# Kernel tuning notes

Hardware: AMD Instinct MI355X
Metric: run time of the kernel (lower is better)

## Reference

```python
import jax, jax.numpy as jnp
import numpy as np
import math

DIMS = 128
VOXEL_SIZE = 4.0
QUANT_SIZE = 0.02
QUANT_LEN = int((2 * VOXEL_SIZE + 0.0001) // QUANT_SIZE)  # 400
N = 1024


def setup_inputs() -> dict:
    key = jax.random.key(0)
    k1, k2, k3, k4, k5, k6 = jax.random.split(key, 6)
    features = jax.random.normal(k1, (N, DIMS), dtype=jnp.float32)
    # distances uniform in [-voxel_size, voxel_size)
    voxel_distances = (jax.random.uniform(k2, (N, N, 3), dtype=jnp.float32) * 2.0 - 1.0) * VOXEL_SIZE
    W_qkv = jax.random.normal(k3, (DIMS, 3 * DIMS), dtype=jnp.float32) * 0.02
    b_qkv = jnp.zeros((3 * DIMS,), dtype=jnp.float32)
    table_x = jax.random.normal(k4, (3, QUANT_LEN, DIMS), dtype=jnp.float32) * 0.02
    table_y = jax.random.normal(k5, (3, QUANT_LEN, DIMS), dtype=jnp.float32) * 0.02
    table_z = jax.random.normal(k6, (3, QUANT_LEN, DIMS), dtype=jnp.float32) * 0.02
    return {"features": features, "voxel_distances": voxel_distances,
            "W_qkv": W_qkv, "b_qkv": b_qkv,
            "table_x": table_x, "table_y": table_y, "table_z": table_z}


def reference(features, voxel_distances, W_qkv, b_qkv, table_x, table_y, table_z):
    n, dims = features.shape
    qkv = (features @ W_qkv + b_qkv).reshape(n, 3, dims)
    q, k, v = qkv[:, 0], qkv[:, 1], qkv[:, 2]  # each [N, D]

    # quantized distance indices, clamped like torch's .clamp(max=...)
    max_idx = VOXEL_SIZE * 2.0 / QUANT_SIZE - 1.0  # 399
    idx = jnp.floor((voxel_distances + VOXEL_SIZE) / QUANT_SIZE)
    idx = jnp.clip(idx, 0.0, max_idx).astype(jnp.int32)  # [N, N, 3]

    # gathered positional encoding: [N, N, D]
    encode_k = table_x[1][idx[:, :, 0]] + table_y[1][idx[:, :, 1]] + table_z[1][idx[:, :, 2]]
    # bias[i, j] = k[i] . encode_k[i, j]  (faithful to k[:, None] @ encode_k^T)
    position_bias = jnp.einsum('id,ijd->ij', k, encode_k)

    scores = (q @ k.T + position_bias) / math.sqrt(dims)
    attn = jax.nn.softmax(scores, axis=-1)  # [N, N]
    return attn @ v  # [N, D]
```

## Files before the change

kernel.cpp:

```cpp
#include <hip/hip_runtime.h>
#include <math.h>

#define N_PTS 1024
#define D 128
#define QL 400
#define PLD 1200
#define SQRT_D_INV 0.08838834764831845f

typedef __attribute__((ext_vector_type(8))) short bf16x8;
typedef __attribute__((ext_vector_type(4))) float f32x4;
typedef unsigned short u16;

#define GLOBAL_AS __attribute__((address_space(1)))
#define LDS_AS    __attribute__((address_space(3)))

__device__ __forceinline__ u16 f2bf(float x) {
    union { float f; unsigned u; } v; v.f = x;
    unsigned r = v.u + 0x7fff + ((v.u >> 16) & 1);
    return (u16)(r >> 16);
}
__device__ __forceinline__ float b2f(u16 h) {
    union { unsigned u; float f; } v; v.u = ((unsigned)h) << 16;
    return v.f;
}

__global__ __launch_bounds__(256) void prep2_kernel(
    const float* __restrict__ features, const float* __restrict__ W,
    const float* __restrict__ bias,
    const float* __restrict__ tx, const float* __restrict__ ty,
    const float* __restrict__ tz,
    u16* __restrict__ qb, u16* __restrict__ kb, u16* __restrict__ vT,
    u16* __restrict__ Pb, unsigned* __restrict__ cnt)
{
    __shared__ __align__(16) u16 smem[24704];
    const int tid = threadIdx.x;
    const int bx = blockIdx.x;
    const int wave = tid >> 6, lane = tid & 63;
    const int wr = wave >> 1, wc = wave & 1;
    const int l15 = lane & 15, l4 = lane >> 4;

    if (bx == 0 && tid < 64) cnt[tid] = 0u;

    if (bx < 96) {
        u16* As = smem;
        u16* Bs = smem + 8192;
        const int bm = (bx / 6) * 64;
        const int bn = (bx % 6) * 64;

        #pragma unroll
        for (int r0 = 0; r0 < 4; ++r0) {
            int unit = r0 * 256 + tid;
            int row = unit >> 4, c16 = unit & 15;
            const float* ga = features + (size_t)(bm + row) * D + c16 * 8;
            float4 a0 = *(const float4*)ga;
            float4 a1 = *(const float4*)(ga + 4);
            u16 h[8] = {f2bf(a0.x), f2bf(a0.y), f2bf(a0.z), f2bf(a0.w),
                        f2bf(a1.x), f2bf(a1.y), f2bf(a1.z), f2bf(a1.w)};
            *(bf16x8*)(As + row * 128 + ((c16 ^ (row & 7)) * 8)) = *(bf16x8*)h;
        }
        #pragma unroll
        for (int r2 = 0; r2 < 8; ++r2) {
            int k = r2 * 16 + (tid >> 4);
            int nl = (tid & 15) * 4;
            float4 w4 = *(const float4*)&W[(size_t)k * 384 + bn + nl];
            float wv[4] = {w4.x, w4.y, w4.z, w4.w};
            #pragma unroll
            for (int e = 0; e < 4; ++e) {
                int n = nl + e;
                Bs[n * 128 + (((k >> 3) ^ (n & 7)) << 3) + (k & 7)] = f2bf(wv[e]);
            }
        }
        __syncthreads();

        f32x4 acc[2][2] = {};
        #pragma unroll
        for (int ks = 0; ks < 4; ++ks) {
            bf16x8 a[2], b[2];
            #pragma unroll
            for (int m = 0; m < 2; ++m) {
                int row = wr * 32 + m * 16 + l15;
                int c16 = ks * 4 + l4;
                a[m] = *(const bf16x8*)(As + row * 128 + ((c16 ^ (row & 7)) * 8));
            }
            #pragma unroll
            for (int n = 0; n < 2; ++n) {
                int row = wc * 32 + n * 16 + l15;
                int c16 = ks * 4 + l4;
                b[n] = *(const bf16x8*)(Bs + row * 128 + ((c16 ^ (row & 7)) * 8));
            }
            #pragma unroll
            for (int m = 0; m < 2; ++m)
                #pragma unroll
                for (int n = 0; n < 2; ++n)
                    acc[m][n] = __builtin_amdgcn_mfma_f32_16x16x32_bf16(
                        a[m], b[n], acc[m][n], 0, 0, 0);
        }

        #pragma unroll
        for (int m = 0; m < 2; ++m)
            #pragma unroll
            for (int n = 0; n < 2; ++n)
                #pragma unroll
                for (int r = 0; r < 4; ++r) {
                    int grow = bm + wr * 32 + m * 16 + l4 * 4 + r;
                    int gcol = bn + wc * 32 + n * 16 + l15;
                    float val = acc[m][n][r] + bias[gcol];
                    int reg = gcol >> 7, lc = gcol & 127;
                    if (reg == 0)      qb[grow * D + lc] = f2bf(val * SQRT_D_INV);
                    else if (reg == 1) kb[grow * D + lc] = f2bf(val);
                    else               vT[(size_t)lc * N_PTS + grow] = f2bf(val);
                }
        return;
    }

    const int t = bx - 96;
    const int ib = t / 19, jb = t % 19;
    const int bm = ib * 64, bn = jb * 64;
    u16* Ta = smem;
    u16* Wb = smem + 8192;
    float* bPl = (float*)(smem + 24576);

    #pragma unroll
    for (int r0 = 0; r0 < 4; ++r0) {
        int unit = r0 * 256 + tid;
        int row = unit >> 4, c16 = unit & 15;
        int c = bn + row; if (c > PLD - 1) c = PLD - 1;
        int sec = c / QL, rr = c - sec * QL;
        const float* tsec = (sec == 0) ? tx : ((sec == 1) ? ty : tz);
        const float* ga = tsec + QL * D + rr * D + c16 * 8;
        float4 a0 = *(const float4*)ga;
        float4 a1 = *(const float4*)(ga + 4);
        u16 h[8] = {f2bf(a0.x), f2bf(a0.y), f2bf(a0.z), f2bf(a0.w),
                    f2bf(a1.x), f2bf(a1.y), f2bf(a1.z), f2bf(a1.w)};
        *(bf16x8*)(Ta + row * 128 + ((c16 ^ (row & 7)) * 8)) = *(bf16x8*)h;
    }
    #pragma unroll
    for (int r0 = 0; r0 < 8; ++r0) {
        int unit = r0 * 256 + tid;
        int e = unit >> 4, c16 = unit & 15;
        const float* ga = W + (size_t)e * 384 + 128 + c16 * 8;
        float4 a0 = *(const float4*)ga;
        float4 a1 = *(const float4*)(ga + 4);
        u16 h[8] = {f2bf(a0.x), f2bf(a0.y), f2bf(a0.z), f2bf(a0.w),
                    f2bf(a1.x), f2bf(a1.y), f2bf(a1.z), f2bf(a1.w)};
        *(bf16x8*)(Wb + e * 128 + ((c16 ^ (e & 7)) * 8)) = *(bf16x8*)h;
    }
    __syncthreads();

    f32x4 accG[2][4] = {};
    #pragma unroll
    for (int ks = 0; ks < 4; ++ks) {
        bf16x8 a[2], bfr[4];
        #pragma unroll
        for (int m = 0; m < 2; ++m) {
            int row = wr * 32 + m * 16 + l15;
            int c16 = ks * 4 + l4;
            a[m] = *(const bf16x8*)(Ta + row * 128 + ((c16 ^ (row & 7)) * 8));
        }
        #pragma unroll
        for (int n = 0; n < 4; ++n) {
            int e = wc * 64 + n * 16 + l15;
            int c16 = ks * 4 + l4;
            bfr[n] = *(const bf16x8*)(Wb + e * 128 + ((c16 ^ (e & 7)) * 8));
        }
        #pragma unroll
        for (int m = 0; m < 2; ++m)
            #pragma unroll
            for (int n = 0; n < 4; ++n)
                accG[m][n] = __builtin_amdgcn_mfma_f32_16x16x32_bf16(
                    a[m], bfr[n], accG[m][n], 0, 0, 0);
    }

    float bsum = 0.0f;
    {
        int c_l = tid >> 2, q = tid & 3;
        #pragma unroll
        for (int dd = 0; dd < 32; ++dd) {
            int d = q * 32 + dd;
            u16 tv = Ta[c_l * 128 + (((d >> 3) ^ (c_l & 7)) * 8) + (d & 7)];
            bsum += b2f(tv) * bias[128 + d];
        }
        bsum += __shfl_xor(bsum, 1);
        bsum += __shfl_xor(bsum, 2);
    }
    __syncthreads();

    #pragma unroll
    for (int m = 0; m < 2; ++m)
        #pragma unroll
        for (int n = 0; n < 4; ++n)
            #pragma unroll
            for (int rr = 0; rr < 4; ++rr) {
                int c_l = wr * 32 + m * 16 + l4 * 4 + rr;
                int e   = wc * 64 + n * 16 + l15;
                Wb[c_l * 128 + (((e >> 3) ^ (c_l & 7)) * 8) + (e & 7)] =
                    f2bf(accG[m][n][rr]);
            }
    #pragma unroll
    for (int r0 = 0; r0 < 4; ++r0) {
        int unit = r0 * 256 + tid;
        int row = unit >> 4, c16 = unit & 15;
        const float* ga = features + (size_t)(bm + row) * D + c16 * 8;
        float4 a0 = *(const float4*)ga;
        float4 a1 = *(const float4*)(ga + 4);
        u16 h[8] = {f2bf(a0.x), f2bf(a0.y), f2bf(a0.z), f2bf(a0.w),
                    f2bf(a1.x), f2bf(a1.y), f2bf(a1.z), f2bf(a1.w)};
        *(bf16x8*)(Ta + row * 128 + ((c16 ^ (row & 7)) * 8)) = *(bf16x8*)h;
    }
    if ((tid & 3) == 0) bPl[tid >> 2] = bsum;
    __syncthreads();

    f32x4 acc[2][2] = {};
    #pragma unroll
    for (int ks = 0; ks < 4; ++ks) {
        bf16x8 a[2], bq[2];
        #pragma unroll
        for (int m = 0; m < 2; ++m) {
            int row = wr * 32 + m * 16 + l15;
            int c16 = ks * 4 + l4;
            a[m] = *(const bf16x8*)(Ta + row * 128 + ((c16 ^ (row & 7)) * 8));
        }
        #pragma unroll
        for (int n = 0; n < 2; ++n) {
            int crow = wc * 32 + n * 16 + l15;
            int c16 = ks * 4 + l4;
            bq[n] = *(const bf16x8*)(Wb + crow * 128 + ((c16 ^ (crow & 7)) * 8));
        }
        #pragma unroll
        for (int m = 0; m < 2; ++m)
            #pragma unroll
            for (int n = 0; n < 2; ++n)
                acc[m][n] = __builtin_amdgcn_mfma_f32_16x16x32_bf16(
                    a[m], bq[n], acc[m][n], 0, 0, 0);
    }
    #pragma unroll
    for (int m = 0; m < 2; ++m)
        #pragma unroll
        for (int n = 0; n < 2; ++n)
            #pragma unroll
            for (int rr = 0; rr < 4; ++rr) {
                int grow = bm + wr * 32 + m * 16 + l4 * 4 + rr;
                int gcol = bn + wc * 32 + n * 16 + l15;
                int c_l  = wc * 32 + n * 16 + l15;
                if (gcol < PLD)
                    Pb[(size_t)grow * PLD + gcol] =
                        f2bf((acc[m][n][rr] + bPl[c_l]) * SQRT_D_INV);
            }
}

__global__ __launch_bounds__(256) void flash_kernel(
    const u16* __restrict__ qb,
    const u16* __restrict__ kb,
    const u16* __restrict__ vT,
    const u16* __restrict__ Pb,
    const float* __restrict__ vd,
    float* __restrict__ part,
    float* __restrict__ rowsumC,
    unsigned* __restrict__ cnt,
    float* __restrict__ out)
{
    __shared__ __align__(16) u16 Pl[2432 * 8];
    __shared__ __align__(16) u16 Ps[16 * 128];
    __shared__ float rsw[4][16];
    __shared__ int lastflag;
    const int tid = threadIdx.x;
    const int wave = tid >> 6, lane = tid & 63;
    const int l15 = lane & 15, l4 = lane >> 4;
    const int it = blockIdx.x;
    const int chunk = blockIdx.y;
    const int bm = it * 16;
    const int bn = chunk * 128;

    const u16* Pg = Pb + (size_t)bm * PLD;
    #pragma unroll
    for (int r0 = 0; r0 < 9; ++r0) {
        int unit = r0 * 256 + tid;
        __builtin_amdgcn_global_load_lds(
            (const GLOBAL_AS unsigned int*)(Pg + unit * 8),
            (LDS_AS unsigned int*)(Pl + r0 * 2048 + wave * 512), 16, 0, 0);
    }
    if (wave < 2) {
        int unit = 9 * 256 + tid;
        int cu = unit > 2399 ? 2399 : unit;
        __builtin_amdgcn_global_load_lds(
            (const GLOBAL_AS unsigned int*)(Pg + cu * 8),
            (LDS_AS unsigned int*)(Pl + 9 * 2048 + wave * 512), 16, 0, 0);
    }

    float vx[2][4], vy[2][4], vz[2][4];
    #pragma unroll
    for (int nn = 0; nn < 2; ++nn)
        #pragma unroll
        for (int r = 0; r < 4; ++r) {
            int i = l4 * 4 + r;
            int j = wave * 32 + nn * 16 + l15;
            const float* vp = vd + ((size_t)(bm + i) * N_PTS + bn + j) * 3;
            vx[nn][r] = vp[0]; vy[nn][r] = vp[1]; vz[nn][r] = vp[2];
        }

    bf16x8 aq[4];
    #pragma unroll
    for (int ks = 0; ks < 4; ++ks)
        aq[ks] = *(const bf16x8*)(qb + (size_t)(bm + l15) * D + ks * 32 + l4 * 8);
    f32x4 acc[2] = {};
    #pragma unroll
    for (int nn = 0; nn < 2; ++nn) {
        int jt = bn + wave * 32 + nn * 16;
        #pragma unroll
        for (int ks = 0; ks < 4; ++ks) {
            bf16x8 bk = *(const bf16x8*)(kb + (size_t)(jt + l15) * D + ks * 32 + l4 * 8);
            acc[nn] = __builtin_amdgcn_mfma_f32_16x16x32_bf16(aq[ks], bk, acc[nn], 0, 0, 0);
        }
    }
    __syncthreads();

    float rs[4] = {0.f, 0.f, 0.f, 0.f};
    #pragma unroll
    for (int nn = 0; nn < 2; ++nn)
        #pragma unroll
        for (int r = 0; r < 4; ++r) {
            int i = l4 * 4 + r;
            int jl = wave * 32 + nn * 16 + l15;
            int ix = (int)floorf((vx[nn][r] + 4.0f) * 50.0f);
            int iy = (int)floorf((vy[nn][r] + 4.0f) * 50.0f);
            int iz = (int)floorf((vz[nn][r] + 4.0f) * 50.0f);
            ix = min(max(ix, 0), QL - 1);
            iy = min(max(iy, 0), QL - 1);
            iz = min(max(iz, 0), QL - 1);
            const u16* Pr = Pl + i * PLD;
            float bv = b2f(Pr[ix]) + b2f(Pr[QL + iy]) + b2f(Pr[2 * QL + iz]);
            float e = __expf(acc[nn][r] + bv);
            rs[r] += e;
            Ps[i * 128 + (((jl >> 3) ^ (i & 7)) * 8) + (jl & 7)] = f2bf(e);
        }
    #pragma unroll
    for (int r = 0; r < 4; ++r)
        #pragma unroll
        for (int off = 1; off < 16; off <<= 1)
            rs[r] += __shfl_xor(rs[r], off);
    if (l15 == 0)
        #pragma unroll
        for (int r = 0; r < 4; ++r) rsw[wave][l4 * 4 + r] = rs[r];
    __syncthreads();
    if (tid < 16)
        rowsumC[(it * 8 + chunk) * 16 + tid] =
            rsw[0][tid] + rsw[1][tid] + rsw[2][tid] + rsw[3][tid];

    bf16x8 pa[4];
    #pragma unroll
    for (int kt = 0; kt < 4; ++kt)
        pa[kt] = *(const bf16x8*)(Ps + l15 * 128 + (((kt * 4 + l4) ^ (l15 & 7)) * 8));
    f32x4 acc2[2] = {};
    #pragma unroll
    for (int nn = 0; nn < 2; ++nn) {
        int dt = wave * 32 + nn * 16;
        #pragma unroll
        for (int kt = 0; kt < 4; ++kt) {
            bf16x8 bv8 = *(const bf16x8*)(vT + (size_t)(dt + l15) * N_PTS + bn + kt * 32 + l4 * 8);
            acc2[nn] = __builtin_amdgcn_mfma_f32_16x16x32_bf16(pa[kt], bv8, acc2[nn], 0, 0, 0);
        }
    }
    float* po = part + (size_t)(it * 8 + chunk) * (16 * D);
    #pragma unroll
    for (int nn = 0; nn < 2; ++nn)
        #pragma unroll
        for (int r = 0; r < 4; ++r)
            po[(l4 * 4 + r) * D + wave * 32 + nn * 16 + l15] = acc2[nn][r];

    asm volatile("s_waitcnt vmcnt(0)" ::: "memory");
    __syncthreads();
    if (tid == 0) {
        unsigned old = __hip_atomic_fetch_add(
            &cnt[it], 1u, __ATOMIC_RELAXED, __HIP_MEMORY_SCOPE_AGENT);
        lastflag = (old == 7u);
    }
    __syncthreads();
    if (lastflag) {
        const float4* p4 = (const float4*)(part + (size_t)it * 8 * 16 * D);
        const float* rsb = rowsumC + it * 8 * 16;
        #pragma unroll
        for (int h = 0; h < 2; ++h) {
            int f4 = h * 256 + tid;
            int row = f4 >> 5;
            float rsum = 0.0f;
            #pragma unroll
            for (int z = 0; z < 8; ++z) rsum += rsb[z * 16 + row];
            float inv = 1.0f / rsum;
            float4 a = p4[f4];
            #pragma unroll
            for (int z = 1; z < 8; ++z) {
                float4 v = p4[z * 512 + f4];
                a.x += v.x; a.y += v.y; a.z += v.z; a.w += v.w;
            }
            a.x *= inv; a.y *= inv; a.z *= inv; a.w *= inv;
            ((float4*)out)[bm * 32 + f4] = a;
        }
    }
}

extern "C" void kernel_launch(void* const* d_in, const int* in_sizes, int n_in,
                              void* d_out, int out_size, void* d_ws, size_t ws_size,
                              hipStream_t stream)
{
    const float* features = (const float*)d_in[0];
    const float* vd       = (const float*)d_in[1];
    const float* W        = (const float*)d_in[2];
    const float* b        = (const float*)d_in[3];
    const float* tx       = (const float*)d_in[4];
    const float* ty       = (const float*)d_in[5];
    const float* tz       = (const float*)d_in[6];
    float* out = (float*)d_out;

    char* w0 = (char*)d_ws;
    unsigned* cnt = (unsigned*)w0;
    u16* qb       = (u16*)(w0 + 0x1000);
    u16* kb       = (u16*)(w0 + 0x50000);
    u16* vT       = (u16*)(w0 + 0x90000);
    u16* Pb       = (u16*)(w0 + 0xD0000);
    float* part   = (float*)(w0 + 0x330000);
    float* rowsumC= (float*)(w0 + 0x730000);

    dim3 blk(256);

    prep2_kernel<<<dim3(400), blk, 0, stream>>>(
        features, W, b, tx, ty, tz, qb, kb, vT, Pb, cnt);

    flash_kernel<<<dim3(64, 8), blk, 0, stream>>>(
        qb, kb, vT, Pb, vd, part, rowsumC, cnt, out);
}
```

Baseline: 23.85 us.

## Double waves per flash block and halve QKV GEMM tile rows

```diff
diff --git a/kernel.cpp b/kernel.cpp
--- a/kernel.cpp
+++ b/kernel.cpp
@@ -41,14 +41,14 @@
 
     if (bx == 0 && tid < 64) cnt[tid] = 0u;
 
-    if (bx < 96) {
+    if (bx < 192) {
         u16* As = smem;
-        u16* Bs = smem + 8192;
-        const int bm = (bx / 6) * 64;
+        u16* Bs = smem + 4096;
+        const int bm = (bx / 6) * 32;
         const int bn = (bx % 6) * 64;
 
         #pragma unroll
-        for (int r0 = 0; r0 < 4; ++r0) {
+        for (int r0 = 0; r0 < 2; ++r0) {
             int unit = r0 * 256 + tid;
             int row = unit >> 4, c16 = unit & 15;
             const float* ga = features + (size_t)(bm + row) * D + c16 * 8;
@@ -72,48 +72,40 @@
         }
         __syncthreads();
 
-        f32x4 acc[2][2] = {};
+        f32x4 acc[2] = {};
         #pragma unroll
         for (int ks = 0; ks < 4; ++ks) {
-            bf16x8 a[2], b[2];
-            #pragma unroll
-            for (int m = 0; m < 2; ++m) {
-                int row = wr * 32 + m * 16 + l15;
-                int c16 = ks * 4 + l4;
-                a[m] = *(const bf16x8*)(As + row * 128 + ((c16 ^ (row & 7)) * 8));
-            }
+            bf16x8 a, b[2];
+            int arow = wr * 16 + l15;
+            int c16 = ks * 4 + l4;
+            a = *(const bf16x8*)(As + arow * 128 + ((c16 ^ (arow & 7)) * 8));
             #pragma unroll
             for (int n = 0; n < 2; ++n) {
                 int row = wc * 32 + n * 16 + l15;
-                int c16 = ks * 4 + l4;
                 b[n] = *(const bf16x8*)(Bs + row * 128 + ((c16 ^ (row & 7)) * 8));
             }
             #pragma unroll
-            for (int m = 0; m < 2; ++m)
-                #pragma unroll
-                for (int n = 0; n < 2; ++n)
-                    acc[m][n] = __builtin_amdgcn_mfma_f32_16x16x32_bf16(
-                        a[m], b[n], acc[m][n], 0, 0, 0);
-        }
-
-        #pragma unroll
-        for (int m = 0; m < 2; ++m)
-            #pragma unroll
             for (int n = 0; n < 2; ++n)
-                #pragma unroll
-                for (int r = 0; r < 4; ++r) {
-                    int grow = bm + wr * 32 + m * 16 + l4 * 4 + r;
-                    int gcol = bn + wc * 32 + n * 16 + l15;
-                    float val = acc[m][n][r] + bias[gcol];
-                    int reg = gcol >> 7, lc = gcol & 127;
-                    if (reg == 0)      qb[grow * D + lc] = f2bf(val * SQRT_D_INV);
-                    else if (reg == 1) kb[grow * D + lc] = f2bf(val);
-                    else               vT[(size_t)lc * N_PTS + grow] = f2bf(val);
-                }
+                acc[n] = __builtin_amdgcn_mfma_f32_16x16x32_bf16(
+                    a, b[n], acc[n], 0, 0, 0);
+        }
+
+        #pragma unroll
+        for (int n = 0; n < 2; ++n)
+            #pragma unroll
+            for (int r = 0; r < 4; ++r) {
+                int grow = bm + wr * 16 + l4 * 4 + r;
+                int gcol = bn + wc * 32 + n * 16 + l15;
+                float val = acc[n][r] + bias[gcol];
+                int reg = gcol >> 7, lc = gcol & 127;
+                if (reg == 0)      qb[grow * D + lc] = f2bf(val * SQRT_D_INV);
+                else if (reg == 1) kb[grow * D + lc] = f2bf(val);
+                else               vT[(size_t)lc * N_PTS + grow] = f2bf(val);
+            }
         return;
     }
 
-    const int t = bx - 96;
+    const int t = bx - 192;
     const int ib = t / 19, jb = t % 19;
     const int bm = ib * 64, bn = jb * 64;
     u16* Ta = smem;
@@ -248,7 +240,7 @@
             }
 }
 
-__global__ __launch_bounds__(256) void flash_kernel(
+__global__ __launch_bounds__(512) void flash_kernel(
     const u16* __restrict__ qb,
     const u16* __restrict__ kb,
     const u16* __restrict__ vT,
@@ -259,12 +251,12 @@
     unsigned* __restrict__ cnt,
     float* __restrict__ out)
 {
-    __shared__ __align__(16) u16 Pl[2432 * 8];
+    __shared__ __align__(16) u16 Pl[2560 * 8];
     __shared__ __align__(16) u16 Ps[16 * 128];
-    __shared__ float rsw[4][16];
+    __shared__ float rsw[8][16];
     __shared__ int lastflag;
     const int tid = threadIdx.x;
-    const int wave = tid >> 6, lane = tid & 63;
+    const int w = tid >> 6, lane = tid & 63;
     const int l15 = lane & 15, l4 = lane >> 4;
     const int it = blockIdx.x;
     const int chunk = blockIdx.y;
@@ -273,66 +265,55 @@
 
     const u16* Pg = Pb + (size_t)bm * PLD;
     #pragma unroll
-    for (int r0 = 0; r0 < 9; ++r0) {
-        int unit = r0 * 256 + tid;
-        __builtin_amdgcn_global_load_lds(
-            (const GLOBAL_AS unsigned int*)(Pg + unit * 8),
-            (LDS_AS unsigned int*)(Pl + r0 * 2048 + wave * 512), 16, 0, 0);
-    }
-    if (wave < 2) {
-        int unit = 9 * 256 + tid;
+    for (int r0 = 0; r0 < 5; ++r0) {
+        int unit = r0 * 512 + tid;
         int cu = unit > 2399 ? 2399 : unit;
         __builtin_amdgcn_global_load_lds(
             (const GLOBAL_AS unsigned int*)(Pg + cu * 8),
-            (LDS_AS unsigned int*)(Pl + 9 * 2048 + wave * 512), 16, 0, 0);
-    }
-
-    float vx[2][4], vy[2][4], vz[2][4];
-    #pragma unroll
-    for (int nn = 0; nn < 2; ++nn)
-        #pragma unroll
-        for (int r = 0; r < 4; ++r) {
-            int i = l4 * 4 + r;
-            int j = wave * 32 + nn * 16 + l15;
-            const float* vp = vd + ((size_t)(bm + i) * N_PTS + bn + j) * 3;
-            vx[nn][r] = vp[0]; vy[nn][r] = vp[1]; vz[nn][r] = vp[2];
-        }
+            (LDS_AS unsigned int*)(Pl + r0 * 4096 + w * 512), 16, 0, 0);
+    }
+
+    float vx[4], vy[4], vz[4];
+    #pragma unroll
+    for (int r = 0; r < 4; ++r) {
+        int i = l4 * 4 + r;
+        int j = bn + w * 16 + l15;
+        const float* vp = vd + ((size_t)(bm + i) * N_PTS + j) * 3;
+        vx[r] = vp[0]; vy[r] = vp[1]; vz[r] = vp[2];
+    }
 
     bf16x8 aq[4];
     #pragma unroll
     for (int ks = 0; ks < 4; ++ks)
         aq[ks] = *(const bf16x8*)(qb + (size_t)(bm + l15) * D + ks * 32 + l4 * 8);
-    f32x4 acc[2] = {};
-    #pragma unroll
-    for (int nn = 0; nn < 2; ++nn) {
-        int jt = bn + wave * 32 + nn * 16;
+    f32x4 acc = {};
+    {
+        int jt = bn + w * 16;
         #pragma unroll
         for (int ks = 0; ks < 4; ++ks) {
             bf16x8 bk = *(const bf16x8*)(kb + (size_t)(jt + l15) * D + ks * 32 + l4 * 8);
-            acc[nn] = __builtin_amdgcn_mfma_f32_16x16x32_bf16(aq[ks], bk, acc[nn], 0, 0, 0);
-        }
-    }
-    __syncthreads();
-
-    float rs[4] = {0.f, 0.f, 0.f, 0.f};
-    #pragma unroll
-    for (int nn = 0; nn < 2; ++nn)
-        #pragma unroll
-        for (int r = 0; r < 4; ++r) {
-            int i = l4 * 4 + r;
-            int jl = wave * 32 + nn * 16 + l15;
-            int ix = (int)floorf((vx[nn][r] + 4.0f) * 50.0f);
-            int iy = (int)floorf((vy[nn][r] + 4.0f) * 50.0f);
-            int iz = (int)floorf((vz[nn][r] + 4.0f) * 50.0f);
-            ix = min(max(ix, 0), QL - 1);
-            iy = min(max(iy, 0), QL - 1);
-            iz = min(max(iz, 0), QL - 1);
-            const u16* Pr = Pl + i * PLD;
-            float bv = b2f(Pr[ix]) + b2f(Pr[QL + iy]) + b2f(Pr[2 * QL + iz]);
-            float e = __expf(acc[nn][r] + bv);
-            rs[r] += e;
-            Ps[i * 128 + (((jl >> 3) ^ (i & 7)) * 8) + (jl & 7)] = f2bf(e);
-        }
+            acc = __builtin_amdgcn_mfma_f32_16x16x32_bf16(aq[ks], bk, acc, 0, 0, 0);
+        }
+    }
+    __syncthreads();
+
+    float rs[4];
+    #pragma unroll
+    for (int r = 0; r < 4; ++r) {
+        int i = l4 * 4 + r;
+        int jl = w * 16 + l15;
+        int ix = (int)floorf((vx[r] + 4.0f) * 50.0f);
+        int iy = (int)floorf((vy[r] + 4.0f) * 50.0f);
+        int iz = (int)floorf((vz[r] + 4.0f) * 50.0f);
+        ix = min(max(ix, 0), QL - 1);
+        iy = min(max(iy, 0), QL - 1);
+        iz = min(max(iz, 0), QL - 1);
+        const u16* Pr = Pl + i * PLD;
+        float bv = b2f(Pr[ix]) + b2f(Pr[QL + iy]) + b2f(Pr[2 * QL + iz]);
+        float e = __expf(acc[r] + bv);
+        rs[r] = e;
+        Ps[i * 128 + (((jl >> 3) ^ (i & 7)) * 8) + (jl & 7)] = f2bf(e);
+    }
     #pragma unroll
     for (int r = 0; r < 4; ++r)
         #pragma unroll
@@ -340,32 +321,27 @@
             rs[r] += __shfl_xor(rs[r], off);
     if (l15 == 0)
         #pragma unroll
-        for (int r = 0; r < 4; ++r) rsw[wave][l4 * 4 + r] = rs[r];
-    __syncthreads();
-    if (tid < 16)
-        rowsumC[(it * 8 + chunk) * 16 + tid] =
-            rsw[0][tid] + rsw[1][tid] + rsw[2][tid] + rsw[3][tid];
-
-    bf16x8 pa[4];
-    #pragma unroll
-    for (int kt = 0; kt < 4; ++kt)
-        pa[kt] = *(const bf16x8*)(Ps + l15 * 128 + (((kt * 4 + l4) ^ (l15 & 7)) * 8));
-    f32x4 acc2[2] = {};
-    #pragma unroll
-    for (int nn = 0; nn < 2; ++nn) {
-        int dt = wave * 32 + nn * 16;
-        #pragma unroll
-        for (int kt = 0; kt < 4; ++kt) {
-            bf16x8 bv8 = *(const bf16x8*)(vT + (size_t)(dt + l15) * N_PTS + bn + kt * 32 + l4 * 8);
-            acc2[nn] = __builtin_amdgcn_mfma_f32_16x16x32_bf16(pa[kt], bv8, acc2[nn], 0, 0, 0);
-        }
+        for (int r = 0; r < 4; ++r) rsw[w][l4 * 4 + r] = rs[r];
+    __syncthreads();
+    if (tid < 16) {
+        float s = 0.0f;
+        #pragma unroll
+        for (int z = 0; z < 8; ++z) s += rsw[z][tid];
+        rowsumC[(it * 8 + chunk) * 16 + tid] = s;
+    }
+
+    const int dt = w * 16;
+    f32x4 acc2 = {};
+    #pragma unroll
+    for (int kt = 0; kt < 4; ++kt) {
+        bf16x8 pa = *(const bf16x8*)(Ps + l15 * 128 + (((kt * 4 + l4) ^ (l15 & 7)) * 8));
+        bf16x8 bv8 = *(const bf16x8*)(vT + (size_t)(dt + l15) * N_PTS + bn + kt * 32 + l4 * 8);
+        acc2 = __builtin_amdgcn_mfma_f32_16x16x32_bf16(pa, bv8, acc2, 0, 0, 0);
     }
     float* po = part + (size_t)(it * 8 + chunk) * (16 * D);
     #pragma unroll
-    for (int nn = 0; nn < 2; ++nn)
-        #pragma unroll
-        for (int r = 0; r < 4; ++r)
-            po[(l4 * 4 + r) * D + wave * 32 + nn * 16 + l15] = acc2[nn][r];
+    for (int r = 0; r < 4; ++r)
+        po[(l4 * 4 + r) * D + dt + l15] = acc2[r];
 
     asm volatile("s_waitcnt vmcnt(0)" ::: "memory");
     __syncthreads();
@@ -378,23 +354,20 @@
     if (lastflag) {
         const float4* p4 = (const float4*)(part + (size_t)it * 8 * 16 * D);
         const float* rsb = rowsumC + it * 8 * 16;
-        #pragma unroll
-        for (int h = 0; h < 2; ++h) {
-            int f4 = h * 256 + tid;
-            int row = f4 >> 5;
-            float rsum = 0.0f;
-            #pragma unroll
-            for (int z = 0; z < 8; ++z) rsum += rsb[z * 16 + row];
-            float inv = 1.0f / rsum;
-            float4 a = p4[f4];
-            #pragma unroll
-            for (int z = 1; z < 8; ++z) {
-                float4 v = p4[z * 512 + f4];
-                a.x += v.x; a.y += v.y; a.z += v.z; a.w += v.w;
-            }
-            a.x *= inv; a.y *= inv; a.z *= inv; a.w *= inv;
-            ((float4*)out)[bm * 32 + f4] = a;
-        }
+        int f4 = tid;
+        int row = f4 >> 5;
+        float rsum = 0.0f;
+        #pragma unroll
+        for (int z = 0; z < 8; ++z) rsum += rsb[z * 16 + row];
+        float inv = 1.0f / rsum;
+        float4 a = p4[f4];
+        #pragma unroll
+        for (int z = 1; z < 8; ++z) {
+            float4 v = p4[z * 512 + f4];
+            a.x += v.x; a.y += v.y; a.z += v.z; a.w += v.w;
+        }
+        a.x *= inv; a.y *= inv; a.z *= inv; a.w *= inv;
+        ((float4*)out)[bm * 32 + f4] = a;
     }
 }
 
@@ -420,11 +393,9 @@
     float* part   = (float*)(w0 + 0x330000);
     float* rowsumC= (float*)(w0 + 0x730000);
 
-    dim3 blk(256);
-
-    prep2_kernel<<<dim3(400), blk, 0, stream>>>(
+    prep2_kernel<<<dim3(496), dim3(256), 0, stream>>>(
         features, W, b, tx, ty, tz, qb, kb, vT, Pb, cnt);
 
-    flash_kernel<<<dim3(64, 8), blk, 0, stream>>>(
+    flash_kernel<<<dim3(64, 8), dim3(512), 0, stream>>>(
         qb, kb, vT, Pb, vd, part, rowsumC, cnt, out);
 }
```

Result: slower. 25.25 us (+5.9%).
